# Performance work log

Measured on AMD Instinct MI355X. Metric: run time of the kernel, lower is better.

Reference implementation:

```python
import jax, jax.numpy as jnp
import numpy as np

P = 7  # corr_size
P2 = P * P
NEG_SLOPE = 0.01  # default LeakyReLU


def _correlate(f1, f2):
    """spatial_correlation_sample with kernel_size=1, stride=1, padding=0,
    dilation_patch=1: out[b,pi,pj,y,x] = sum_c f1[b,c,y,x] * f2[b,c,y+pi-r,x+pj-r]
    (zero padded), returned flattened to [b, P*P, h, w]."""
    r = P // 2
    b, c, h, w = f1.shape
    f2p = jnp.pad(f2, ((0, 0), (0, 0), (r, r), (r, r)))
    outs = []
    for pi in range(P):
        for pj in range(P):
            sh = jax.lax.slice(f2p, (0, 0, pi, pj), (b, c, pi + h, pj + w))
            outs.append(jnp.sum(f1 * sh, axis=1))  # [b,h,w]
    return jnp.stack(outs, axis=1)  # [b, P*P, h, w]


def _conv3x3(x, w, b):
    y = jax.lax.conv_general_dilated(
        x, w, window_strides=(1, 1), padding=((1, 1), (1, 1)),
        dimension_numbers=('NCHW', 'OIHW', 'NCHW'))
    return y + b[None, :, None, None]


def _up_nearest(x, s):
    return jnp.repeat(jnp.repeat(x, s, axis=2), s, axis=3)


def _level(feat1, feat2, h_pre, c_pre, w, b, scale):
    # feat1 = current frame (x), feat2 = previous frame (x_pre)
    u1 = _up_nearest(feat1, scale)
    u2 = _up_nearest(feat2, scale)
    corr = _correlate(u1, u2)                        # [B, P*P, H*s, W*s]
    corr = jnp.where(corr >= 0, corr, NEG_SLOPE * corr)  # leaky relu
    dw = corr[:, :, ::scale, ::scale]                # nearest downsample back
    lstm_in = jnp.concatenate([dw, h_pre], axis=1)   # [B, 2*P*P, H, W]
    conv = _conv3x3(lstm_in, w, b)                   # [B, 4*P*P, H, W]
    cc_i, cc_f, cc_o, cc_g = jnp.split(conv, 4, axis=1)
    i = jax.nn.sigmoid(cc_i)
    f = jax.nn.sigmoid(cc_f)
    o = jax.nn.sigmoid(cc_o)
    g = jnp.tanh(cc_g)
    c_next = f * c_pre + i * g
    h_next = o * jnp.tanh(c_next)
    return h_next, c_next


def setup_inputs() -> dict:
    key = jax.random.key(0)
    ks = jax.random.split(key, 10)
    x0 = jax.random.normal(ks[0], (2, 512, 64, 64), jnp.float32) * 0.1
    x1 = jax.random.normal(ks[1], (2, 1024, 32, 32), jnp.float32) * 0.1
    xp0 = jax.random.normal(ks[2], (2, 512, 64, 64), jnp.float32) * 0.1
    xp1 = jax.random.normal(ks[3], (2, 1024, 32, 32), jnp.float32) * 0.1
    h0 = jax.random.normal(ks[4], (2, P2, 64, 64), jnp.float32) * 0.1
    c0 = jax.random.normal(ks[5], (2, P2, 64, 64), jnp.float32) * 0.1
    h1 = jax.random.normal(ks[6], (2, P2, 32, 32), jnp.float32) * 0.1
    c1 = jax.random.normal(ks[7], (2, P2, 32, 32), jnp.float32) * 0.1
    w0 = jax.random.normal(ks[8], (4 * P2, 2 * P2, 3, 3), jnp.float32) * 0.02
    w1 = jax.random.normal(ks[9], (4 * P2, 2 * P2, 3, 3), jnp.float32) * 0.02
    # init_weights sets the forget-gate bias slice to 1
    b0 = jnp.zeros((4 * P2,), jnp.float32).at[P2:2 * P2].set(1.0)
    b1 = jnp.zeros((4 * P2,), jnp.float32).at[P2:2 * P2].set(1.0)
    return {"x0": x0, "x1": x1, "xp0": xp0, "xp1": xp1,
            "h0": h0, "c0": c0, "h1": h1, "c1": c1,
            "w0": w0, "b0": b0, "w1": w1, "b1": b1}


def reference(x0, x1, xp0, xp1, h0, c0, h1, c1, w0, b0, w1, b1):
    # level i: upsample scale = upsample_param * 2**i = 2 * 2**i
    h0n, c0n = _level(x0, xp0, h0, c0, w0, b0, scale=2)
    h1n, c1n = _level(x1, xp1, h1, c1, w1, b1, scale=4)
    return (h0n, c0n, h1n, c1n)
```

## Files before the change

### kernel.cpp

```cpp
#include <hip/hip_runtime.h>

#define DEVFN __device__ __forceinline__

typedef __attribute__((ext_vector_type(8))) __bf16 bf16x8;
typedef __attribute__((ext_vector_type(16))) float f32x16;
typedef unsigned short ushort;

DEVFN float sigmoidf_(float x) { return 1.f / (1.f + __expf(-x)); }

DEVFN ushort f2bf(float f) {
    unsigned u = __float_as_uint(f);
    unsigned r = (u + 0x7FFF + ((u >> 16) & 1)) >> 16;
    return (ushort)r;
}

template<int C, int CC, int H, int W, int NOFF, int OFS, int UNR>
__global__ void corr_kernel(const float* __restrict__ f1, const float* __restrict__ f2,
                            float* __restrict__ slices) {
    constexpr int HW = H * W;
    constexpr bool NEEDHI = (NOFF - 1 - OFS) >= 1;
    const int t     = threadIdx.x;
    const int px    = blockIdx.x * 1024 + t * 4;
    const int b     = blockIdx.y;
    const int chunk = blockIdx.z;
    const int y  = px / W;
    const int x0 = px - y * W;

    const float* f1p = f1 + ((size_t)b * C + chunk * CC) * HW + px;
    const float* f2b = f2 + ((size_t)b * C + chunk * CC) * HW;

    float acc[NOFF][NOFF][4];
#pragma unroll
    for (int i = 0; i < NOFF; ++i)
#pragma unroll
        for (int j = 0; j < NOFF; ++j)
#pragma unroll
            for (int p = 0; p < 4; ++p) acc[i][j][p] = 0.f;

#pragma unroll UNR
    for (int c = 0; c < CC; ++c) {
        float f1a[4];
        *reinterpret_cast<float4*>(f1a) = *reinterpret_cast<const float4*>(f1p + (size_t)c * HW);
        const float* f2c = f2b + (size_t)c * HW;
#pragma unroll
        for (int dyi = 0; dyi < NOFF; ++dyi) {
            const int yy = y + dyi - OFS;
            const bool rv = (yy >= 0) && (yy < H);
            const float* rp = f2c + yy * W + x0;
            float w[12];
            float4 z = make_float4(0.f, 0.f, 0.f, 0.f);
            float4 lo  = (rv && x0 >= 4)    ? *reinterpret_cast<const float4*>(rp - 4) : z;
            float4 mid = rv                 ? *reinterpret_cast<const float4*>(rp)     : z;
            float4 hi  = (NEEDHI && rv && (x0 + 4 < W)) ? *reinterpret_cast<const float4*>(rp + 4) : z;
            *reinterpret_cast<float4*>(&w[0]) = lo;
            *reinterpret_cast<float4*>(&w[4]) = mid;
            *reinterpret_cast<float4*>(&w[8]) = hi;
#pragma unroll
            for (int dxi = 0; dxi < NOFF; ++dxi)
#pragma unroll
                for (int p = 0; p < 4; ++p)
                    acc[dyi][dxi][p] = fmaf(f1a[p], w[4 + p + dxi - OFS], acc[dyi][dxi][p]);
        }
    }

    float* ao = slices + ((size_t)(chunk * 2 + b) * NOFF * NOFF) * HW + px;
#pragma unroll
    for (int dyi = 0; dyi < NOFF; ++dyi)
#pragma unroll
        for (int dxi = 0; dxi < NOFF; ++dxi)
            *reinterpret_cast<float4*>(ao + (size_t)(dyi * NOFF + dxi) * HW) =
                make_float4(acc[dyi][dxi][0], acc[dyi][dxi][1], acc[dyi][dxi][2], acc[dyi][dxi][3]);
}

template<int S, int STRIDE>
__global__ void reduce_kernel(const float* __restrict__ in, float* __restrict__ out) {
    const int i = (blockIdx.x * 256 + threadIdx.x) * 4;
    if (i >= STRIDE) return;
    float sx = 0.f, sy = 0.f, sz = 0.f, sw = 0.f;
#pragma unroll 8
    for (int k = 0; k < S; ++k) {
        float4 v = *reinterpret_cast<const float4*>(in + (size_t)k * STRIDE + i);
        sx += v.x; sy += v.y; sz += v.z; sw += v.w;
    }
    *reinterpret_cast<float4*>(out + i) = make_float4(sx, sy, sz, sw);
}

template<int H, int W, int SCALE, int SHIFT, int NOFF, int OFS>
__global__ void xbuild_kernel(const float* __restrict__ base, const float* __restrict__ h_pre,
                              ushort* __restrict__ Xin) {
    const int HW = H * W;
    int i = blockIdx.x * 256 + threadIdx.x;
    if (i >= 2 * HW * 16) return;
    int g  = i & 15;
    int px = (i >> 4) % HW;
    int b  = (i >> 4) / HW;
    int y = px / W, x = px - y * W;
    ushort out8[8];
#pragma unroll
    for (int j = 0; j < 8; ++j) {
        int ic = g * 8 + j;
        float v = 0.f;
        if (ic < 49) {
            int pi = ic / 7, pj = ic - pi * 7;
            int dy = pi - 3, dx = pj - 3;
            int uy = SCALE * y + dy, ux = SCALE * x + dx;
            if (uy >= 0 && uy < SCALE * H && ux >= 0 && ux < SCALE * W) {
                int idy = (dy >> SHIFT) + OFS;
                int idx = (dx >> SHIFT) + OFS;
                float cv = base[((size_t)b * NOFF * NOFF + idy * NOFF + idx) * HW + px];
                v = cv >= 0.f ? cv : 0.01f * cv;
            }
        } else if (ic < 98) {
            v = h_pre[((size_t)b * 49 + (ic - 49)) * HW + px];
        }
        out8[j] = f2bf(v);
    }
    *reinterpret_cast<uint4*>(Xin + (size_t)i * 8) = *reinterpret_cast<uint4*>(out8);
}

__global__ void wprep_kernel(const float* __restrict__ w0, const float* __restrict__ w1,
                             ushort* __restrict__ Wmf0, ushort* __restrict__ Wmf1) {
    const float* w = blockIdx.y ? w1 : w0;
    ushort* Wmf    = blockIdx.y ? Wmf1 : Wmf0;
    int i = blockIdx.x * 256 + threadIdx.x;
    const int n = 9 * 16 * 256 * 8;
    if (i >= n) return;
    int iEl = i & 7;
    int oc  = (i >> 3) & 255;
    int icg = (i >> 11) & 15;
    int tap = i >> 15;
    int ic  = icg * 8 + iEl;
    float v = (oc < 196 && ic < 98) ? w[((size_t)oc * 98 + ic) * 9 + tap] : 0.f;
    Wmf[i] = f2bf(v);
}

template<int H, int W, int SPLIT, int ICPS, int NKC, int STRIDE>
__global__ void convmf_kernel(const ushort* __restrict__ Xin, const ushort* __restrict__ Wmf,
                              float* __restrict__ Y) {
    const int HW = H * W;
    __shared__ ushort Xs[180 * STRIDE];
    const int tilesx = W / 16;
    const int by0 = (blockIdx.x / tilesx) * 8;
    const int bx0 = (blockIdx.x % tilesx) * 16;
    const int ocb = blockIdx.y * 64;
    const int b   = blockIdx.z & 1;
    const int s   = blockIdx.z >> 1;
    const int t   = threadIdx.x;
    const int wv  = t >> 6;
    const int l   = t & 63;
    const int G   = ICPS / 8;

    for (int u = t; u < 180 * G; u += 256) {
        int px = u / G, g = u - px * G;
        int gy = by0 + px / 18 - 1;
        int gx = bx0 + px % 18 - 1;
        uint4 v = make_uint4(0u, 0u, 0u, 0u);
        if (gy >= 0 && gy < H && gx >= 0 && gx < W)
            v = *reinterpret_cast<const uint4*>(Xin + (((size_t)b * HW + gy * W + gx) * 128 + s * ICPS + g * 8));
        *reinterpret_cast<uint4*>(&Xs[px * STRIDE + g * 8]) = v;
    }
    __syncthreads();

    f32x16 acc0 = {};
    f32x16 acc1 = {};
    const int n    = l & 31;
    const int hi   = l >> 5;
    const int wrow = 2 * wv + (n >> 4);
    const int wcol = n & 15;

#pragma unroll 1
    for (int kc = 0; kc < NKC; ++kc) {
        bf16x8 af[2][9];
        const int icg = (s * ICPS + kc * 16) / 8 + hi;
        const ushort* wp = Wmf + ((size_t)icg * 256 + ocb + n) * 8;
#pragma unroll
        for (int j = 0; j < 9; ++j) {
            af[0][j] = *reinterpret_cast<const bf16x8*>(wp + (size_t)j * 16 * 256 * 8);
            af[1][j] = *reinterpret_cast<const bf16x8*>(wp + (size_t)j * 16 * 256 * 8 + 32 * 8);
        }
#pragma unroll
        for (int j = 0; j < 9; ++j) {
            const int ky = j / 3, kx = j - (j / 3) * 3;
            const int hp = (wrow + ky) * 18 + wcol + kx;
            bf16x8 bf = *reinterpret_cast<const bf16x8*>(&Xs[hp * STRIDE + kc * 16 + hi * 8]);
            acc0 = __builtin_amdgcn_mfma_f32_32x32x16_bf16(af[0][j], bf, acc0, 0, 0, 0);
            acc1 = __builtin_amdgcn_mfma_f32_32x32x16_bf16(af[1][j], bf, acc1, 0, 0, 0);
        }
    }

    float* Yo = Y + ((size_t)(s * 2 + b) * 196) * HW;
    const int po = (by0 + wrow) * W + bx0 + wcol;
#pragma unroll
    for (int r = 0; r < 16; ++r) {
        int m = (r & 3) + 8 * (r >> 2) + 4 * hi;
        int oc0 = ocb + m;
        if (oc0 < 196) Yo[(size_t)oc0 * HW + po] = acc0[r];
        int oc1 = ocb + 32 + m;
        if (oc1 < 196) Yo[(size_t)oc1 * HW + po] = acc1[r];
    }
}

template<int S, int HW>
__global__ void lstm_kernel(const float* __restrict__ Y, const float* __restrict__ bias,
                            const float* __restrict__ c_pre,
                            float* __restrict__ h_out, float* __restrict__ c_out) {
    int i = blockIdx.x * 256 + threadIdx.x;
    const int n = 2 * 49 * HW;
    if (i >= n) return;
    int b   = i / (49 * HW);
    int rem = i - b * (49 * HW);
    int k   = rem / HW;
    float g4[4];
#pragma unroll
    for (int gi = 0; gi < 4; ++gi) {
        float v = bias[gi * 49 + k];
#pragma unroll
        for (int ss = 0; ss < S; ++ss)
            v += Y[((size_t)((ss * 2 + b) * 196) + gi * 49) * HW + rem];
        g4[gi] = v;
    }
    float iv = sigmoidf_(g4[0]);
    float fv = sigmoidf_(g4[1]);
    float ov = sigmoidf_(g4[2]);
    float gv = tanhf(g4[3]);
    float cp = c_pre[i];
    float cn = fv * cp + iv * gv;
    h_out[i] = ov * tanhf(cn);
    c_out[i] = cn;
}

extern "C" void kernel_launch(void* const* d_in, const int* in_sizes, int n_in,
                              void* d_out, int out_size, void* d_ws, size_t ws_size,
                              hipStream_t stream) {
    (void)in_sizes; (void)n_in; (void)out_size; (void)ws_size;
    const float* x0  = (const float*)d_in[0];
    const float* x1  = (const float*)d_in[1];
    const float* xp0 = (const float*)d_in[2];
    const float* xp1 = (const float*)d_in[3];
    const float* h0  = (const float*)d_in[4];
    const float* c0  = (const float*)d_in[5];
    const float* h1  = (const float*)d_in[6];
    const float* c1  = (const float*)d_in[7];
    const float* w0  = (const float*)d_in[8];
    const float* b0  = (const float*)d_in[9];
    const float* w1  = (const float*)d_in[10];
    const float* b1  = (const float*)d_in[11];
    float* out = (float*)d_out;

    float* ws = (float*)d_ws;
    float*  Wmf0f = ws;
    float*  Wmf1f = Wmf0f + 147456;
    float*  Xin0f = Wmf1f + 147456;
    float*  Xin1f = Xin0f + 524288;
    float*  base0 = Xin1f + 131072;
    float*  base1 = base0 + 131072;
    float*  Y0    = base1 + 8192;
    float*  Y1    = Y0 + 3211264;
    float*  slc0  = Y0;
    float*  slc1  = Y0 + 4194304;
    ushort* Wmf0 = (ushort*)Wmf0f;
    ushort* Wmf1 = (ushort*)Wmf1f;
    ushort* Xin0 = (ushort*)Xin0f;
    ushort* Xin1 = (ushort*)Xin1f;

    corr_kernel<512, 16, 64, 64, 4, 2, 2><<<dim3(4, 2, 32), 256, 0, stream>>>(x0, xp0, slc0);
    corr_kernel<1024, 16, 32, 32, 2, 1, 4><<<dim3(1, 2, 64), 256, 0, stream>>>(x1, xp1, slc1);

    reduce_kernel<32, 131072><<<128, 256, 0, stream>>>(slc0, base0);
    reduce_kernel<64, 8192><<<8, 256, 0, stream>>>(slc1, base1);

    wprep_kernel<<<dim3(1152, 2), 256, 0, stream>>>(w0, w1, Wmf0, Wmf1);

    xbuild_kernel<64, 64, 2, 1, 4, 2><<<512, 256, 0, stream>>>(base0, h0, Xin0);
    xbuild_kernel<32, 32, 4, 2, 2, 1><<<128, 256, 0, stream>>>(base1, h1, Xin1);

    convmf_kernel<64, 64, 2, 64, 4, 72><<<dim3(32, 4, 4), 256, 0, stream>>>(Xin0, Wmf0, Y0);
    convmf_kernel<32, 32, 4, 32, 2, 40><<<dim3(8, 4, 8), 256, 0, stream>>>(Xin1, Wmf1, Y1);

    lstm_kernel<2, 4096><<<1568, 256, 0, stream>>>(Y0, b0, c0, out + 0,      out + 401408);
    lstm_kernel<4, 1024><<<392,  256, 0, stream>>>(Y1, b1, c1, out + 802816, out + 903168);
}
```

Before: 221.4 us.

## Double-buffer correlation loads and read conv inputs directly from channel-blocked global layout

The correlation kernel now precomputes row pointers and validity once, trims the f2 window to only the needed columns, and software-pipelines channel loads with FMAs through two register buffers. The conv input tensor is re-laid out into 16-channel blocks per pixel. The MFMA conv kernel now reads its B fragments straight from global memory instead of staging a halo tile in LDS behind a barrier. Both kernels gain launch bounds for two blocks per CU. The trade is fewer LDS stores and syncs against redundant, cache-dependent global reads of halo pixels.

Result: slower. 317.6 us (+43.4%).

```diff
diff --git a/kernel.cpp b/kernel.cpp
--- a/kernel.cpp
+++ b/kernel.cpp
@@ -14,11 +14,12 @@
     return (ushort)r;
 }
 
-template<int C, int CC, int H, int W, int NOFF, int OFS, int UNR>
-__global__ void corr_kernel(const float* __restrict__ f1, const float* __restrict__ f2,
-                            float* __restrict__ slices) {
+template<int C, int CC, int H, int W, int NOFF, int OFS>
+__global__ __launch_bounds__(256, 2) void corr_kernel(const float* __restrict__ f1,
+                                                      const float* __restrict__ f2,
+                                                      float* __restrict__ slices) {
     constexpr int HW = H * W;
-    constexpr bool NEEDHI = (NOFF - 1 - OFS) >= 1;
+    constexpr int WINSZ = NOFF + 3;
     const int t     = threadIdx.x;
     const int px    = blockIdx.x * 1024 + t * 4;
     const int b     = blockIdx.y;
@@ -29,6 +30,16 @@
     const float* f1p = f1 + ((size_t)b * C + chunk * CC) * HW + px;
     const float* f2b = f2 + ((size_t)b * C + chunk * CC) * HW;
 
+    bool rv[NOFF]; const float* rp[NOFF];
+#pragma unroll
+    for (int d = 0; d < NOFF; ++d) {
+        int yy = y + d - OFS;
+        rv[d] = (yy >= 0) && (yy < H);
+        rp[d] = f2b + (size_t)(rv[d] ? yy : 0) * W + x0;
+    }
+    const bool lok = x0 >= 4;
+    const bool hok = (x0 + 4) < W;
+
     float acc[NOFF][NOFF][4];
 #pragma unroll
     for (int i = 0; i < NOFF; ++i)
@@ -37,31 +48,44 @@
 #pragma unroll
             for (int p = 0; p < 4; ++p) acc[i][j][p] = 0.f;
 
-#pragma unroll UNR
-    for (int c = 0; c < CC; ++c) {
-        float f1a[4];
-        *reinterpret_cast<float4*>(f1a) = *reinterpret_cast<const float4*>(f1p + (size_t)c * HW);
-        const float* f2c = f2b + (size_t)c * HW;
-#pragma unroll
-        for (int dyi = 0; dyi < NOFF; ++dyi) {
-            const int yy = y + dyi - OFS;
-            const bool rv = (yy >= 0) && (yy < H);
-            const float* rp = f2c + yy * W + x0;
-            float w[12];
-            float4 z = make_float4(0.f, 0.f, 0.f, 0.f);
-            float4 lo  = (rv && x0 >= 4)    ? *reinterpret_cast<const float4*>(rp - 4) : z;
-            float4 mid = rv                 ? *reinterpret_cast<const float4*>(rp)     : z;
-            float4 hi  = (NEEDHI && rv && (x0 + 4 < W)) ? *reinterpret_cast<const float4*>(rp + 4) : z;
-            *reinterpret_cast<float4*>(&w[0]) = lo;
-            *reinterpret_cast<float4*>(&w[4]) = mid;
-            *reinterpret_cast<float4*>(&w[8]) = hi;
-#pragma unroll
-            for (int dxi = 0; dxi < NOFF; ++dxi)
-#pragma unroll
-                for (int p = 0; p < 4; ++p)
-                    acc[dyi][dxi][p] = fmaf(f1a[p], w[4 + p + dxi - OFS], acc[dyi][dxi][p]);
-        }
-    }
+#define CORR_LOAD(cc_, F1V, WIN) {                                                            \
+    *reinterpret_cast<float4*>(F1V) = *reinterpret_cast<const float4*>(f1p + (size_t)(cc_) * HW); \
+    _Pragma("unroll")                                                                         \
+    for (int d_ = 0; d_ < NOFF; ++d_) {                                                       \
+        const float* r_ = rp[d_] + (size_t)(cc_) * HW;                                        \
+        const float4 z4_ = make_float4(0.f, 0.f, 0.f, 0.f);                                   \
+        if constexpr (OFS == 2) {                                                             \
+            float4 lo_ = (rv[d_] && lok) ? *reinterpret_cast<const float4*>(r_ - 4) : z4_;    \
+            float4 md_ = rv[d_] ? *reinterpret_cast<const float4*>(r_) : z4_;                 \
+            float  hv_ = (rv[d_] && hok) ? r_[4] : 0.f;                                       \
+            WIN[d_][0] = lo_.z; WIN[d_][1] = lo_.w; WIN[d_][2] = md_.x; WIN[d_][3] = md_.y;   \
+            WIN[d_][4] = md_.z; WIN[d_][5] = md_.w; WIN[d_][6] = hv_;                         \
+        } else {                                                                              \
+            float  lv_ = (rv[d_] && lok) ? r_[-1] : 0.f;                                      \
+            float4 md_ = rv[d_] ? *reinterpret_cast<const float4*>(r_) : z4_;                 \
+            WIN[d_][0] = lv_; WIN[d_][1] = md_.x; WIN[d_][2] = md_.y; WIN[d_][3] = md_.z;     \
+            WIN[d_][4] = md_.w;                                                               \
+        }                                                                                     \
+    } }
+
+#define CORR_FMA(F1V, WIN) {                                                                  \
+    _Pragma("unroll") for (int d_ = 0; d_ < NOFF; ++d_)                                       \
+    _Pragma("unroll") for (int dx_ = 0; dx_ < NOFF; ++dx_)                                    \
+    _Pragma("unroll") for (int p_ = 0; p_ < 4; ++p_)                                          \
+        acc[d_][dx_][p_] = fmaf(F1V[p_], WIN[d_][p_ + dx_], acc[d_][dx_][p_]); }
+
+    float f1A[4], f1B[4];
+    float winA[NOFF][WINSZ], winB[NOFF][WINSZ];
+    CORR_LOAD(0, f1A, winA);
+#pragma unroll
+    for (int c = 0; c < CC; c += 2) {
+        if (c + 1 < CC) CORR_LOAD(c + 1, f1B, winB);
+        CORR_FMA(f1A, winA);
+        if (c + 2 < CC) CORR_LOAD(c + 2, f1A, winA);
+        if (c + 1 < CC) CORR_FMA(f1B, winB);
+    }
+#undef CORR_LOAD
+#undef CORR_FMA
 
     float* ao = slices + ((size_t)(chunk * 2 + b) * NOFF * NOFF) * HW + px;
 #pragma unroll
@@ -115,7 +139,8 @@
         }
         out8[j] = f2bf(v);
     }
-    *reinterpret_cast<uint4*>(Xin + (size_t)i * 8) = *reinterpret_cast<uint4*>(out8);
+    size_t off = (((size_t)b * 8 + (g >> 1)) * HW + px) * 16 + (g & 1) * 8;
+    *reinterpret_cast<uint4*>(Xin + off) = *reinterpret_cast<uint4*>(out8);
 }
 
 __global__ void wprep_kernel(const float* __restrict__ w0, const float* __restrict__ w1,
@@ -134,11 +159,11 @@
     Wmf[i] = f2bf(v);
 }
 
-template<int H, int W, int SPLIT, int ICPS, int NKC, int STRIDE>
-__global__ void convmf_kernel(const ushort* __restrict__ Xin, const ushort* __restrict__ Wmf,
-                              float* __restrict__ Y) {
+template<int H, int W, int SPLIT, int ICPS, int NKC>
+__global__ __launch_bounds__(256, 2) void convmf_kernel(const ushort* __restrict__ Xin,
+                                                        const ushort* __restrict__ Wmf,
+                                                        float* __restrict__ Y) {
     const int HW = H * W;
-    __shared__ ushort Xs[180 * STRIDE];
     const int tilesx = W / 16;
     const int by0 = (blockIdx.x / tilesx) * 8;
     const int bx0 = (blockIdx.x % tilesx) * 16;
@@ -148,43 +173,32 @@
     const int t   = threadIdx.x;
     const int wv  = t >> 6;
     const int l   = t & 63;
-    const int G   = ICPS / 8;
-
-    for (int u = t; u < 180 * G; u += 256) {
-        int px = u / G, g = u - px * G;
-        int gy = by0 + px / 18 - 1;
-        int gx = bx0 + px % 18 - 1;
-        uint4 v = make_uint4(0u, 0u, 0u, 0u);
-        if (gy >= 0 && gy < H && gx >= 0 && gx < W)
-            v = *reinterpret_cast<const uint4*>(Xin + (((size_t)b * HW + gy * W + gx) * 128 + s * ICPS + g * 8));
-        *reinterpret_cast<uint4*>(&Xs[px * STRIDE + g * 8]) = v;
-    }
-    __syncthreads();
-
-    f32x16 acc0 = {};
-    f32x16 acc1 = {};
     const int n    = l & 31;
     const int hi   = l >> 5;
     const int wrow = 2 * wv + (n >> 4);
     const int wcol = n & 15;
 
-#pragma unroll 1
+    f32x16 acc0 = {};
+    f32x16 acc1 = {};
+
+#pragma unroll
     for (int kc = 0; kc < NKC; ++kc) {
-        bf16x8 af[2][9];
-        const int icg = (s * ICPS + kc * 16) / 8 + hi;
-        const ushort* wp = Wmf + ((size_t)icg * 256 + ocb + n) * 8;
+        const int icg8  = (s * ICPS + kc * 16) / 8 + hi;
+        const int icg16 = (s * ICPS) / 16 + kc;
+        const ushort* wp = Wmf + ((size_t)icg8 * 256 + ocb + n) * 8;
+        const ushort* xb = Xin + ((size_t)b * 8 + icg16) * HW * 16 + hi * 8;
 #pragma unroll
         for (int j = 0; j < 9; ++j) {
-            af[0][j] = *reinterpret_cast<const bf16x8*>(wp + (size_t)j * 16 * 256 * 8);
-            af[1][j] = *reinterpret_cast<const bf16x8*>(wp + (size_t)j * 16 * 256 * 8 + 32 * 8);
-        }
-#pragma unroll
-        for (int j = 0; j < 9; ++j) {
-            const int ky = j / 3, kx = j - (j / 3) * 3;
-            const int hp = (wrow + ky) * 18 + wcol + kx;
-            bf16x8 bf = *reinterpret_cast<const bf16x8*>(&Xs[hp * STRIDE + kc * 16 + hi * 8]);
-            acc0 = __builtin_amdgcn_mfma_f32_32x32x16_bf16(af[0][j], bf, acc0, 0, 0, 0);
-            acc1 = __builtin_amdgcn_mfma_f32_32x32x16_bf16(af[1][j], bf, acc1, 0, 0, 0);
+            const int ky = j / 3, kx = j - ky * 3;
+            bf16x8 a0 = *reinterpret_cast<const bf16x8*>(wp + (size_t)j * 16 * 256 * 8);
+            bf16x8 a1 = *reinterpret_cast<const bf16x8*>(wp + (size_t)j * 16 * 256 * 8 + 32 * 8);
+            const int gy = by0 + wrow + ky - 1;
+            const int gx = bx0 + wcol + kx - 1;
+            bf16x8 bfr = {};
+            if (gy >= 0 && gy < H && gx >= 0 && gx < W)
+                bfr = *reinterpret_cast<const bf16x8*>(xb + (size_t)(gy * W + gx) * 16);
+            acc0 = __builtin_amdgcn_mfma_f32_32x32x16_bf16(a0, bfr, acc0, 0, 0, 0);
+            acc1 = __builtin_amdgcn_mfma_f32_32x32x16_bf16(a1, bfr, acc1, 0, 0, 0);
         }
     }
 
@@ -263,8 +277,8 @@
     ushort* Xin0 = (ushort*)Xin0f;
     ushort* Xin1 = (ushort*)Xin1f;
 
-    corr_kernel<512, 16, 64, 64, 4, 2, 2><<<dim3(4, 2, 32), 256, 0, stream>>>(x0, xp0, slc0);
-    corr_kernel<1024, 16, 32, 32, 2, 1, 4><<<dim3(1, 2, 64), 256, 0, stream>>>(x1, xp1, slc1);
+    corr_kernel<512, 16, 64, 64, 4, 2><<<dim3(4, 2, 32), 256, 0, stream>>>(x0, xp0, slc0);
+    corr_kernel<1024, 16, 32, 32, 2, 1><<<dim3(1, 2, 64), 256, 0, stream>>>(x1, xp1, slc1);
 
     reduce_kernel<32, 131072><<<128, 256, 0, stream>>>(slc0, base0);
     reduce_kernel<64, 8192><<<8, 256, 0, stream>>>(slc1, base1);
@@ -274,8 +288,8 @@
     xbuild_kernel<64, 64, 2, 1, 4, 2><<<512, 256, 0, stream>>>(base0, h0, Xin0);
     xbuild_kernel<32, 32, 4, 2, 2, 1><<<128, 256, 0, stream>>>(base1, h1, Xin1);
 
-    convmf_kernel<64, 64, 2, 64, 4, 72><<<dim3(32, 4, 4), 256, 0, stream>>>(Xin0, Wmf0, Y0);
-    convmf_kernel<32, 32, 4, 32, 2, 40><<<dim3(8, 4, 8), 256, 0, stream>>>(Xin1, Wmf1, Y1);
+    convmf_kernel<64, 64, 2, 64, 4><<<dim3(32, 4, 4), 256, 0, stream>>>(Xin0, Wmf0, Y0);
+    convmf_kernel<32, 32, 4, 32, 2><<<dim3(8, 4, 8), 256, 0, stream>>>(Xin1, Wmf1, Y1);
 
     lstm_kernel<2, 4096><<<1568, 256, 0, stream>>>(Y0, b0, c0, out + 0,      out + 401408);
     lstm_kernel<4, 1024><<<392,  256, 0, stream>>>(Y1, b1, c1, out + 802816, out + 903168);
```
